# Performance work log

Measured on AMD Instinct MI355X. Metric: run time of the kernel, lower is better.

Reference implementation:

```python
import jax, jax.numpy as jnp
import numpy as np

N_W = 96  # n_workers
N_F = 96  # n_firms


def setup_inputs() -> dict:
    key = jax.random.key(0)
    kw, kf, kr = jax.random.split(key, 3)
    # Each worker ranks the n_firms+1 options (firms + unmatch) with a random permutation,
    # encoded as a one-hot (n_firms+1, n_firms+1) matrix: W[i, j, k] = 1 iff firm j is at rank k.
    pw = jax.vmap(lambda k: jax.random.permutation(k, N_F + 1))(jax.random.split(kw, N_W))
    W = jnp.eye(N_F + 1, dtype=jnp.float32)[pw]                  # (N_W, N_F+1, N_F+1)
    pf = jax.vmap(lambda k: jax.random.permutation(k, N_W + 1))(jax.random.split(kf, N_F))
    F = jnp.eye(N_W + 1, dtype=jnp.float32)[pf]                  # (N_F, N_W+1, N_W+1)
    # R: permutation (dictatorship order) matrix over all workers+firms; column r is one-hot
    # on the agent that dictates in round r.
    perm = jax.random.permutation(kr, N_W + N_F)
    R = jnp.eye(N_W + N_F, dtype=jnp.float32)[perm]              # (N_W+N_F, N_W+N_F)
    return {"W": W, "F": F, "R": R}


def _triangle_window(x):
    # TriangleWindowFunction.forward: x on (0,1], 2-x on (1,2], 0 elsewhere (clamped at 0).
    return jnp.clip(jnp.where(x > 1.0, 2.0 - x, jnp.where(x > 0.0, x, 0.0)), 0.0)


def _find_counterpart(P):
    # first available (rank-first) choice indicator, then map rank -> agent via P.
    first_j = _triangle_window(jnp.cumsum(jnp.sum(P, axis=0)))
    return P @ first_j[:, None]                                  # (n+1, 1)


def _forward(W, F, R):
    n_w, n_f = W.shape[0], F.shape[0]
    dt = W.dtype
    gate_w = jnp.concatenate([jnp.ones((n_f, 1), dt), jnp.zeros((1, 1), dt)])  # zero out unmatch row
    gate_f = jnp.concatenate([jnp.ones((n_w, 1), dt), jnp.zeros((1, 1), dt)])
    zero1 = jnp.zeros((1,), dt)

    def step(carry, ds):
        Wc, Fc, M = carry
        d_w, d_f = ds                                            # (n_w,), (n_f,)
        P_w = jnp.einsum('wij,w->ij', Wc, d_w)                   # dictator-worker's ranking
        P_f = jnp.einsum('fij,f->ij', Fc, d_f)
        c_w = _find_counterpart(P_w)                             # (n_f+1, 1)
        c_f = _find_counterpart(P_f)                             # (n_w+1, 1)
        dw1 = jnp.concatenate([d_w, zero1])                      # (n_w+1,)
        df1 = jnp.concatenate([d_f, zero1])                      # (n_f+1,)
        # matching += M_w + M_f.T
        M = M + dw1[:, None] * c_w[:, 0][None, :] + c_f * df1[None, :]
        # ranking_masks_for_workers[r] has row i = -d_f[i] (0 on unmatch row): equals -df1[:,None].
        # matching_mask_for_workers = -(c_w * gate_w) broadcast across columns.
        Wn = jnp.clip(Wc - c_w * gate_w - df1[:, None], 0.0) * (1.0 - c_f)[:n_w, :, None]
        Fn = jnp.clip(Fc - c_f * gate_f - dw1[:, None], 0.0) * (1.0 - c_w)[:n_f, :, None]
        return (Wn, Fn, M), None

    xs = (R[:n_w].T, R[n_w:].T)                                  # per-round dictator indicators
    M0 = jnp.zeros((n_w + 1, n_f + 1), dt)
    (_, _, M), _ = jax.lax.scan(step, (W, F, M0), xs)
    return M


def reference(W, F, R):
    return _forward(W, F, R)
```

## Files before the change

kernel.cpp:

```cpp
#include <hip/hip_runtime.h>
#include <hip/hip_bf16.h>
#include <stdint.h>

#define N_W 96
#define N_F 96
#define NAG 192
#define NP1 97
#define W_ELEMS (N_W * NP1 * NP1)
#define R_ELEMS (NAG * NAG)
#define WB ((W_ELEMS / 4 + 255) / 256)
#define RB ((R_ELEMS / 4 + 255) / 256)

__global__ __launch_bounds__(256) void decode_kernel(
    const float* __restrict__ W, const float* __restrict__ F,
    const float* __restrict__ R,
    short* __restrict__ ps, short* __restrict__ ord) {
    int b = blockIdx.x;
    if (b < 2 * WB) {
        const float* src = (b < WB) ? W : F;
        int abase = (b < WB) ? 0 : N_W;
        int i4 = (b - ((b < WB) ? 0 : WB)) * 256 + threadIdx.x;
        if (i4 < W_ELEMS / 4) {
            float4 v = ((const float4*)src)[i4];
            int base = i4 * 4;
            #pragma unroll
            for (int u = 0; u < 4; ++u) {
                float x = (u == 0) ? v.x : (u == 1) ? v.y : (u == 2) ? v.z : v.w;
                if (x > 0.5f) {
                    int idx = base + u;
                    int a = idx / (NP1 * NP1);
                    int rem = idx - a * (NP1 * NP1);
                    int j = rem / NP1;
                    int k = rem - j * NP1;
                    int slot = (k < 64) ? (2 * k) : (2 * (k - 64) + 1);
                    ps[(abase + a) * 128 + slot] = (short)j;
                }
            }
        }
    } else {
        int i4 = (b - 2 * WB) * 256 + threadIdx.x;
        if (i4 < R_ELEMS / 4) {
            float4 v = ((const float4*)R)[i4];
            int base = i4 * 4;
            #pragma unroll
            for (int u = 0; u < 4; ++u) {
                float x = (u == 0) ? v.x : (u == 1) ? v.y : (u == 2) ? v.z : v.w;
                if (x > 0.5f) {
                    int idx = base + u;
                    int a = idx / NAG;
                    int r = idx - a * NAG;
                    ord[r] = (short)a;
                }
            }
        }
    }
}

#define LOAD8(dst, rb) \
    dst##0 = s_pko[((rb) << 6) + t];        \
    dst##1 = s_pko[((rb) << 6) + 64 + t];   \
    dst##2 = s_pko[((rb) << 6) + 128 + t];  \
    dst##3 = s_pko[((rb) << 6) + 192 + t];  \
    dst##4 = s_pko[((rb) << 6) + 256 + t];  \
    dst##5 = s_pko[((rb) << 6) + 320 + t];  \
    dst##6 = s_pko[((rb) << 6) + 384 + t];  \
    dst##7 = s_pko[((rb) << 6) + 448 + t];

#define GROUP8(rb, P_) do {                                                 \
    int seg_ = (rb) >> 6;                                                   \
    uint32_t osel_ = (seg_ == 0) ? ordv0 : (seg_ == 1) ? ordv1 : ordv2;     \
    ROUND((rb) + 0, P_##0, osel_);                                          \
    ROUND((rb) + 1, P_##1, osel_);                                          \
    ROUND((rb) + 2, P_##2, osel_);                                          \
    ROUND((rb) + 3, P_##3, osel_);                                          \
    ROUND((rb) + 4, P_##4, osel_);                                          \
    ROUND((rb) + 5, P_##5, osel_);                                          \
    ROUND((rb) + 6, P_##6, osel_);                                          \
    ROUND((rb) + 7, P_##7, osel_);                                          \
} while (0)

template <int MODE>
__global__ __launch_bounds__(256, 1) void sd_kernel(
    const uint32_t* __restrict__ pk_g, const short* __restrict__ ord_g,
    float* __restrict__ out) {
    __shared__ __align__(16) uint32_t s_pko[NAG * 64];
    __shared__ uint32_t s_match[NAG];

    const int t = threadIdx.x;
    const unsigned short* og = (const unsigned short*)ord_g;

    for (int idx = t; idx < NAG * 16; idx += 256) {
        int r = idx >> 4, q = idx & 15;
        int a = (int)og[r];
        ((uint4*)s_pko)[idx] = ((const uint4*)(pk_g + (a << 6)))[q];
    }
    if (t < NAG) s_match[t] = 0xFFFFFFFFu;
    __syncthreads();

    if (MODE == 0) {
        for (int i = t; i < 2352; i += 256)
            ((float4*)out)[i] = ((float4*)s_pko)[i];
        if (t == 0) out[9408] = 0.f;
    } else if (t < 64) {
        uint32_t ordv0 = og[t], ordv1 = og[64 + t], ordv2 = og[128 + t];
        uint64_t rWlo = 0, rWhi = 0, rFlo = 0, rFhi = 0;

        auto ROUND = [&](int r, uint32_t P, uint32_t osel) {
            uint32_t j1 = P & 0xFFFFu, j2 = P >> 16;
            uint32_t s1 = j1 & 63u, s2 = j2 & 63u;
            uint32_t lo1 = (j1 < 64u) ? 1u : 0u;
            uint32_t hi1 = (j1 >= 64u && j1 < 96u) ? 1u : 0u;
            uint32_t lo2 = (j2 < 64u) ? 1u : 0u;
            uint32_t hi2 = (j2 >= 64u && j2 < 96u) ? 1u : 0u;
            int a = __builtin_amdgcn_readlane((int)osel, r & 63);
            if (a < 96) {
                uint64_t own = (a < 64) ? rWlo : rWhi;
                bool dead = ((own >> (a & 63)) & 1ull) != 0ull;
                uint64_t sb = 1ull << (a & 63);
                if (a < 64) rWlo |= sb; else rWhi |= sb;
                if (!dead) {
                    uint32_t bad1 = (((uint32_t)(rFlo >> s1)) & lo1)
                                  | (((uint32_t)(rFhi >> s1)) & hi1);
                    uint32_t bad2 = (((uint32_t)(rFlo >> s2)) & lo2)
                                  | (((uint32_t)(rFhi >> s2)) & hi2);
                    unsigned long long m1 = __ballot(bad1 == 0u);
                    unsigned long long m2 = __ballot(bad2 == 0u);
                    int k = (m1 != 0ull) ? (__ffsll(m1) - 1) : (63 + __ffsll(m2));
                    uint32_t pc = (uint32_t)__builtin_amdgcn_readlane((int)P, k & 63);
                    uint32_t js = (k >= 64) ? (pc >> 16) : (pc & 0xFFFFu);
                    s_match[r] = (uint32_t)(a * NP1 + (int)js);
                    if (js < 96u) {
                        uint64_t cb = 1ull << (js & 63u);
                        if (js < 64u) rFlo |= cb; else rFhi |= cb;
                    }
                }
            } else {
                int aa = a - 96;
                uint64_t own = (aa < 64) ? rFlo : rFhi;
                bool dead = ((own >> (aa & 63)) & 1ull) != 0ull;
                uint64_t sb = 1ull << (aa & 63);
                if (aa < 64) rFlo |= sb; else rFhi |= sb;
                if (!dead) {
                    uint32_t bad1 = (((uint32_t)(rWlo >> s1)) & lo1)
                                  | (((uint32_t)(rWhi >> s1)) & hi1);
                    uint32_t bad2 = (((uint32_t)(rWlo >> s2)) & lo2)
                                  | (((uint32_t)(rWhi >> s2)) & hi2);
                    unsigned long long m1 = __ballot(bad1 == 0u);
                    unsigned long long m2 = __ballot(bad2 == 0u);
                    int k = (m1 != 0ull) ? (__ffsll(m1) - 1) : (63 + __ffsll(m2));
                    uint32_t pc = (uint32_t)__builtin_amdgcn_readlane((int)P, k & 63);
                    uint32_t js = (k >= 64) ? (pc >> 16) : (pc & 0xFFFFu);
                    s_match[r] = (uint32_t)((int)js * NP1 + aa);
                    if (js < 96u) {
                        uint64_t cb = 1ull << (js & 63u);
                        if (js < 64u) rWlo |= cb; else rWhi |= cb;
                    }
                }
            }
        };

        uint32_t Pa0, Pa1, Pa2, Pa3, Pa4, Pa5, Pa6, Pa7;
        uint32_t Pb0, Pb1, Pb2, Pb3, Pb4, Pb5, Pb6, Pb7;
        LOAD8(Pa, 0);
        for (int g = 0; g < 24; g += 2) {
            int rb1 = (g + 1) << 3;
            LOAD8(Pb, rb1);
            GROUP8(g << 3, Pa);
            int g2 = g + 2;
            int rb2 = ((g2 < 24) ? g2 : 23) << 3;
            LOAD8(Pa, rb2);
            GROUP8(rb1, Pb);
        }
    } else {
        for (int i = t - 64; i < 2352; i += 192)
            ((float4*)out)[i] = make_float4(0.f, 0.f, 0.f, 0.f);
        if (t == 64) out[9408] = 0.f;
    }
    __syncthreads();
    if (t < NAG) {
        uint32_t c = s_match[t];
        if (c != 0xFFFFFFFFu) out[c] = 1.0f;
    }
}

extern "C" void kernel_launch(void* const* d_in, const int* in_sizes, int n_in,
                              void* d_out, int out_size, void* d_ws, size_t ws_size,
                              hipStream_t stream) {
    const float* W = (const float*)d_in[0];
    const float* F = (const float*)d_in[1];
    const float* R = (const float*)d_in[2];
    float* out = (float*)d_out;

    uint32_t* packed = (uint32_t*)d_ws;
    short* ord = (short*)((char*)d_ws + NAG * 64 * 4);
    float* diag = (float*)((char*)d_ws + (64 << 10));

    decode_kernel<<<2 * WB + RB, 256, 0, stream>>>(W, F, R, (short*)packed, ord);
    if (ws_size >= (128u << 10))
        sd_kernel<0><<<1, 256, 0, stream>>>(packed, ord, diag);
    sd_kernel<1><<<1, 256, 0, stream>>>(packed, ord, out);
}
```

Measured before the change: 49.42 us.

## Drop diagnostic launch and make serial dictator loop branch-free with uniform order loads

```diff
diff --git a/kernel.cpp b/kernel.cpp
--- a/kernel.cpp
+++ b/kernel.cpp
@@ -66,20 +66,17 @@
     dst##6 = s_pko[((rb) << 6) + 384 + t];  \
     dst##7 = s_pko[((rb) << 6) + 448 + t];
 
-#define GROUP8(rb, P_) do {                                                 \
-    int seg_ = (rb) >> 6;                                                   \
-    uint32_t osel_ = (seg_ == 0) ? ordv0 : (seg_ == 1) ? ordv1 : ordv2;     \
-    ROUND((rb) + 0, P_##0, osel_);                                          \
-    ROUND((rb) + 1, P_##1, osel_);                                          \
-    ROUND((rb) + 2, P_##2, osel_);                                          \
-    ROUND((rb) + 3, P_##3, osel_);                                          \
-    ROUND((rb) + 4, P_##4, osel_);                                          \
-    ROUND((rb) + 5, P_##5, osel_);                                          \
-    ROUND((rb) + 6, P_##6, osel_);                                          \
-    ROUND((rb) + 7, P_##7, osel_);                                          \
+#define GROUP8(rb, P_, ov_) do {                        \
+    ROUND((rb) + 0, P_##0, (int)((ov_).x & 0xFFFFu));   \
+    ROUND((rb) + 1, P_##1, (int)((ov_).x >> 16));       \
+    ROUND((rb) + 2, P_##2, (int)((ov_).y & 0xFFFFu));   \
+    ROUND((rb) + 3, P_##3, (int)((ov_).y >> 16));       \
+    ROUND((rb) + 4, P_##4, (int)((ov_).z & 0xFFFFu));   \
+    ROUND((rb) + 5, P_##5, (int)((ov_).z >> 16));       \
+    ROUND((rb) + 6, P_##6, (int)((ov_).w & 0xFFFFu));   \
+    ROUND((rb) + 7, P_##7, (int)((ov_).w >> 16));       \
 } while (0)
 
-template <int MODE>
 __global__ __launch_bounds__(256, 1) void sd_kernel(
     const uint32_t* __restrict__ pk_g, const short* __restrict__ ord_g,
     float* __restrict__ out) {
@@ -94,83 +91,71 @@
         int a = (int)og[r];
         ((uint4*)s_pko)[idx] = ((const uint4*)(pk_g + (a << 6)))[q];
     }
-    if (t < NAG) s_match[t] = 0xFFFFFFFFu;
     __syncthreads();
 
-    if (MODE == 0) {
-        for (int i = t; i < 2352; i += 256)
-            ((float4*)out)[i] = ((float4*)s_pko)[i];
-        if (t == 0) out[9408] = 0.f;
-    } else if (t < 64) {
-        uint32_t ordv0 = og[t], ordv1 = og[64 + t], ordv2 = og[128 + t];
+    if (t < 64) {
         uint64_t rWlo = 0, rWhi = 0, rFlo = 0, rFhi = 0;
+        uint32_t cell0 = 0xFFFFFFFFu, cell1 = 0xFFFFFFFFu, cell2 = 0xFFFFFFFFu;
 
-        auto ROUND = [&](int r, uint32_t P, uint32_t osel) {
+        auto ROUND = [&](int r, uint32_t P, int a) {
             uint32_t j1 = P & 0xFFFFu, j2 = P >> 16;
             uint32_t s1 = j1 & 63u, s2 = j2 & 63u;
             uint32_t lo1 = (j1 < 64u) ? 1u : 0u;
             uint32_t hi1 = (j1 >= 64u && j1 < 96u) ? 1u : 0u;
             uint32_t lo2 = (j2 < 64u) ? 1u : 0u;
             uint32_t hi2 = (j2 >= 64u && j2 < 96u) ? 1u : 0u;
-            int a = __builtin_amdgcn_readlane((int)osel, r & 63);
-            if (a < 96) {
-                uint64_t own = (a < 64) ? rWlo : rWhi;
-                bool dead = ((own >> (a & 63)) & 1ull) != 0ull;
-                uint64_t sb = 1ull << (a & 63);
-                if (a < 64) rWlo |= sb; else rWhi |= sb;
-                if (!dead) {
-                    uint32_t bad1 = (((uint32_t)(rFlo >> s1)) & lo1)
-                                  | (((uint32_t)(rFhi >> s1)) & hi1);
-                    uint32_t bad2 = (((uint32_t)(rFlo >> s2)) & lo2)
-                                  | (((uint32_t)(rFhi >> s2)) & hi2);
-                    unsigned long long m1 = __ballot(bad1 == 0u);
-                    unsigned long long m2 = __ballot(bad2 == 0u);
-                    int k = (m1 != 0ull) ? (__ffsll(m1) - 1) : (63 + __ffsll(m2));
-                    uint32_t pc = (uint32_t)__builtin_amdgcn_readlane((int)P, k & 63);
-                    uint32_t js = (k >= 64) ? (pc >> 16) : (pc & 0xFFFFu);
-                    s_match[r] = (uint32_t)(a * NP1 + (int)js);
-                    if (js < 96u) {
-                        uint64_t cb = 1ull << (js & 63u);
-                        if (js < 64u) rFlo |= cb; else rFhi |= cb;
-                    }
-                }
-            } else {
-                int aa = a - 96;
-                uint64_t own = (aa < 64) ? rFlo : rFhi;
-                bool dead = ((own >> (aa & 63)) & 1ull) != 0ull;
-                uint64_t sb = 1ull << (aa & 63);
-                if (aa < 64) rFlo |= sb; else rFhi |= sb;
-                if (!dead) {
-                    uint32_t bad1 = (((uint32_t)(rWlo >> s1)) & lo1)
-                                  | (((uint32_t)(rWhi >> s1)) & hi1);
-                    uint32_t bad2 = (((uint32_t)(rWlo >> s2)) & lo2)
-                                  | (((uint32_t)(rWhi >> s2)) & hi2);
-                    unsigned long long m1 = __ballot(bad1 == 0u);
-                    unsigned long long m2 = __ballot(bad2 == 0u);
-                    int k = (m1 != 0ull) ? (__ffsll(m1) - 1) : (63 + __ffsll(m2));
-                    uint32_t pc = (uint32_t)__builtin_amdgcn_readlane((int)P, k & 63);
-                    uint32_t js = (k >= 64) ? (pc >> 16) : (pc & 0xFFFFu);
-                    s_match[r] = (uint32_t)((int)js * NP1 + aa);
-                    if (js < 96u) {
-                        uint64_t cb = 1ull << (js & 63u);
-                        if (js < 64u) rWlo |= cb; else rWhi |= cb;
-                    }
-                }
-            }
+            int isW = (a < 96) ? 1 : 0;
+            int aa  = isW ? a : (a - 96);
+            int sh  = aa & 63;
+            int ahi = aa >> 6;
+            uint64_t sb = 1ull << sh;
+            uint64_t ownlo = isW ? rWlo : rFlo;
+            uint64_t ownhi = isW ? rWhi : rFhi;
+            uint64_t ownw  = ahi ? ownhi : ownlo;
+            uint32_t alive = 1u - ((uint32_t)(ownw >> sh) & 1u);
+            uint64_t slo = ahi ? 0ull : sb;
+            uint64_t shi = ahi ? sb : 0ull;
+            rWlo |= isW ? slo : 0ull;  rWhi |= isW ? shi : 0ull;
+            rFlo |= isW ? 0ull : slo;  rFhi |= isW ? 0ull : shi;
+            uint64_t olo = isW ? rFlo : rWlo;
+            uint64_t ohi = isW ? rFhi : rWhi;
+            uint32_t bad1 = (((uint32_t)(olo >> s1)) & lo1) | (((uint32_t)(ohi >> s1)) & hi1);
+            uint32_t bad2 = (((uint32_t)(olo >> s2)) & lo2) | (((uint32_t)(ohi >> s2)) & hi2);
+            unsigned long long m1 = __ballot(bad1 == 0u);
+            unsigned long long m2 = __ballot(bad2 == 0u) & 0x1FFFFFFFFull;
+            int k = (m1 != 0ull) ? (__ffsll(m1) - 1) : (63 + __ffsll(m2));
+            uint32_t pc = (uint32_t)__builtin_amdgcn_readlane((int)P, k & 63);
+            uint32_t js = (k >= 64) ? (pc >> 16) : (pc & 0xFFFFu);
+            uint32_t take = alive & ((js < 96u) ? 1u : 0u);
+            uint64_t cb = 1ull << (js & 63u);
+            int jhi = (int)(js >> 6);
+            uint64_t clo = (take && !jhi) ? cb : 0ull;
+            uint64_t chi = (take &&  jhi) ? cb : 0ull;
+            rFlo |= isW ? clo : 0ull;  rFhi |= isW ? chi : 0ull;
+            rWlo |= isW ? 0ull : clo;  rWhi |= isW ? 0ull : chi;
+            uint32_t cellu = alive ? (isW ? (uint32_t)(aa * NP1 + (int)js)
+                                          : (uint32_t)((int)js * NP1 + aa))
+                                   : 0xFFFFFFFFu;
+            cell0 = (t == r)       ? cellu : cell0;
+            cell1 = (t == r - 64)  ? cellu : cell1;
+            cell2 = (t == r - 128) ? cellu : cell2;
         };
 
         uint32_t Pa0, Pa1, Pa2, Pa3, Pa4, Pa5, Pa6, Pa7;
         uint32_t Pb0, Pb1, Pb2, Pb3, Pb4, Pb5, Pb6, Pb7;
+        uint4 ovA = ((const uint4*)og)[0];
+        uint4 ovB;
         LOAD8(Pa, 0);
         for (int g = 0; g < 24; g += 2) {
-            int rb1 = (g + 1) << 3;
-            LOAD8(Pb, rb1);
-            GROUP8(g << 3, Pa);
-            int g2 = g + 2;
-            int rb2 = ((g2 < 24) ? g2 : 23) << 3;
-            LOAD8(Pa, rb2);
-            GROUP8(rb1, Pb);
+            ovB = ((const uint4*)og)[g + 1];
+            LOAD8(Pb, (g + 1) << 3);
+            GROUP8(g << 3, Pa, ovA);
+            int g2 = (g + 2 < 24) ? (g + 2) : 23;
+            ovA = ((const uint4*)og)[g2];
+            LOAD8(Pa, g2 << 3);
+            GROUP8((g + 1) << 3, Pb, ovB);
         }
+        s_match[t] = cell0; s_match[64 + t] = cell1; s_match[128 + t] = cell2;
     } else {
         for (int i = t - 64; i < 2352; i += 192)
             ((float4*)out)[i] = make_float4(0.f, 0.f, 0.f, 0.f);
@@ -193,10 +178,7 @@
 
     uint32_t* packed = (uint32_t*)d_ws;
     short* ord = (short*)((char*)d_ws + NAG * 64 * 4);
-    float* diag = (float*)((char*)d_ws + (64 << 10));
 
     decode_kernel<<<2 * WB + RB, 256, 0, stream>>>(W, F, R, (short*)packed, ord);
-    if (ws_size >= (128u << 10))
-        sd_kernel<0><<<1, 256, 0, stream>>>(packed, ord, diag);
-    sd_kernel<1><<<1, 256, 0, stream>>>(packed, ord, out);
+    sd_kernel<<<1, 256, 0, stream>>>(packed, ord, out);
 }
```

Result: slower. 66.62 us (+34.8%).
